# Kernel optimization log

Hardware: AMD Instinct MI355X
Metric: run time of the kernel (lower is better)

The kernel has to match this reference:

```python
import jax, jax.numpy as jnp
import numpy as np

N_NODES = 100000
N_EDGES = 3200000
D_FEAT = 128
HIDDEN = 128
BN_EPS = 1e-3  # Keras BatchNormalization default epsilon


def setup_inputs() -> dict:
    key = jax.random.key(0)
    k = jax.random.split(key, 8)
    H = jax.random.normal(k[0], (N_NODES, D_FEAT), dtype=jnp.float32)
    edge_src = jax.random.randint(k[1], (N_EDGES,), 0, N_NODES, dtype=jnp.int32)
    edge_dst = jax.random.randint(k[2], (N_EDGES,), 0, N_NODES, dtype=jnp.int32)
    edge_w = jax.random.uniform(k[3], (N_EDGES,), dtype=jnp.float32)
    # BatchNorm (inference-mode) parameters
    gamma = jnp.ones((D_FEAT,), dtype=jnp.float32)
    beta = jnp.zeros((D_FEAT,), dtype=jnp.float32)
    moving_mean = 0.1 * jax.random.normal(k[4], (D_FEAT,), dtype=jnp.float32)
    moving_var = jnp.abs(1.0 + 0.1 * jax.random.normal(k[5], (D_FEAT,), dtype=jnp.float32))
    # Dense layer params
    W = jax.random.normal(k[6], (D_FEAT, HIDDEN), dtype=jnp.float32) / np.sqrt(D_FEAT)
    b = jnp.zeros((HIDDEN,), dtype=jnp.float32)
    return {
        "H": H, "edge_src": edge_src, "edge_dst": edge_dst, "edge_w": edge_w,
        "gamma": gamma, "beta": beta, "moving_mean": moving_mean,
        "moving_var": moving_var, "W": W, "b": b, "num_nodes": N_NODES,
    }


def reference(H, edge_src, edge_dst, edge_w, gamma, beta, moving_mean, moving_var, W, b, num_nodes):
    # Sparse adjacency SpMM: h[dst] += w * H[src]
    msgs = H[edge_src] * edge_w[:, None]                      # [E, d]
    h = jax.ops.segment_sum(msgs, edge_dst, num_segments=num_nodes)  # [N, d]
    # BatchNorm (inference) -> Dropout (identity at inference) -> Dense + exact GELU
    h = (h - moving_mean) * jax.lax.rsqrt(moving_var + BN_EPS) * gamma + beta
    out = jax.nn.gelu(h @ W + b, approximate=False)           # [N, hidden]
    return out
```

## Files before the change

### kernel.cpp

```cpp
#include <hip/hip_runtime.h>
#include <math.h>


#define DF 128
#define SCAN_ELEMS 1024
#define BKSH 6
#define BKNODES (1 << BKSH)
#define NB 128
#define CAP 4096
#define CAP2 3072

typedef short short8 __attribute__((ext_vector_type(8)));
typedef float f32x4 __attribute__((ext_vector_type(4)));

__device__ __forceinline__ unsigned short f32_to_bf16_rne(float f) {
  unsigned u = __float_as_uint(f);
  return (unsigned short)((u + 0x7FFFu + ((u >> 16) & 1u)) >> 16);
}

__global__ __launch_bounds__(256) void scatter_kernel(
    const float* __restrict__ H, const int* __restrict__ esrc,
    const int* __restrict__ edst, const float* __restrict__ ew,
    float* __restrict__ h, int E) {
  int tid = blockIdx.x * blockDim.x + threadIdx.x;
  int e = tid >> 5;
  int lane = tid & 31;
  if (e >= E) return;
  int s = esrc[e];
  int d = edst[e];
  float w = ew[e];
  const float4* Hs = reinterpret_cast<const float4*>(H + (size_t)s * DF);
  float4 v = Hs[lane];
  float* hd = h + (size_t)d * DF + lane * 4;
  atomicAdd(hd + 0, v.x * w);
  atomicAdd(hd + 1, v.y * w);
  atomicAdd(hd + 2, v.z * w);
  atomicAdd(hd + 3, v.w * w);
}

__global__ __launch_bounds__(256) void prep_all_kernel(
    const float4* __restrict__ H4, ushort4* __restrict__ Hb, int n4,
    const float* __restrict__ W, const float* __restrict__ gamma,
    const float* __restrict__ beta, const float* __restrict__ mean,
    const float* __restrict__ var, const float* __restrict__ b,
    unsigned short* __restrict__ W2frag, float* __restrict__ bias2) {
  int idx = blockIdx.x * blockDim.x + threadIdx.x;
  if (idx < n4) {
    float4 v = H4[idx];
    ushort4 o;
    o.x = f32_to_bf16_rne(v.x);
    o.y = f32_to_bf16_rne(v.y);
    o.z = f32_to_bf16_rne(v.z);
    o.w = f32_to_bf16_rne(v.w);
    Hb[idx] = o;
  }
  if (idx < 16384) {
    int i = idx & 7;
    int l = (idx >> 3) & 63;
    int kt = (idx >> 9) & 3;
    int ct = idx >> 11;
    int k = kt * 32 + (l >> 4) * 8 + i;
    int c = ct * 16 + (l & 15);
    float s = gamma[k] * rsqrtf(var[k] + 1e-3f);
    W2frag[idx] = f32_to_bf16_rne(s * W[(size_t)k * DF + c]);
  } else if (idx < 16384 + DF) {
    int c = idx - 16384;
    float acc = b[c];
    for (int k = 0; k < DF; ++k) {
      float s = gamma[k] * rsqrtf(var[k] + 1e-3f);
      float t = beta[k] - mean[k] * s;
      acc += t * W[(size_t)k * DF + c];
    }
    bias2[c] = acc;
  }
}

__global__ __launch_bounds__(512) void hist_blk_kernel(
    const int* __restrict__ edst, int* __restrict__ bcnt,
    int E, int nbk, int chunk) {
  extern __shared__ int hcnt[];
  int bblk = blockIdx.x;
  int t = threadIdx.x;
  for (int i = t; i < nbk; i += 512) hcnt[i] = 0;
  __syncthreads();
  int e0 = bblk * chunk;
  int e1 = min(E, e0 + chunk);
  for (int e = e0 + t; e < e1; e += 512)
    atomicAdd(&hcnt[edst[e] >> BKSH], 1);
  __syncthreads();
  for (int k = t; k < nbk; k += 512)
    bcnt[(size_t)k * NB + bblk] = hcnt[k];
}

__global__ __launch_bounds__(256) void scan1_kernel(
    const int* __restrict__ cnt, int* __restrict__ pre,
    int* __restrict__ bsum, int N) {
  __shared__ int s[256];
  int t = threadIdx.x;
  int base = blockIdx.x * SCAN_ELEMS + t * 4;
  int v0 = (base + 0 < N) ? cnt[base + 0] : 0;
  int v1 = (base + 1 < N) ? cnt[base + 1] : 0;
  int v2 = (base + 2 < N) ? cnt[base + 2] : 0;
  int v3 = (base + 3 < N) ? cnt[base + 3] : 0;
  int tsum = v0 + v1 + v2 + v3;
  s[t] = tsum;
  __syncthreads();
  for (int off = 1; off < 256; off <<= 1) {
    int tmp = (t >= off) ? s[t - off] : 0;
    __syncthreads();
    s[t] += tmp;
    __syncthreads();
  }
  int run = s[t] - tsum;
  if (base + 0 < N) pre[base + 0] = run;
  run += v0;
  if (base + 1 < N) pre[base + 1] = run;
  run += v1;
  if (base + 2 < N) pre[base + 2] = run;
  run += v2;
  if (base + 3 < N) pre[base + 3] = run;
  if (t == 255) bsum[blockIdx.x] = s[255];
}

__global__ __launch_bounds__(256) void scan23_kernel(
    int* __restrict__ gbase, const int* __restrict__ bsum, int NBKG, int nbA) {
  __shared__ int s[256];
  int t = threadIdx.x;
  int v = (t < nbA) ? bsum[t] : 0;
  s[t] = v;
  __syncthreads();
  for (int off = 1; off < 256; off <<= 1) {
    int tmp = (t >= off) ? s[t - off] : 0;
    __syncthreads();
    s[t] += tmp;
    __syncthreads();
  }
  int i = blockIdx.x * 256 + t;
  if (i < NBKG) {
    int blk = i >> 10;
    int add = (blk == 0) ? 0 : s[blk - 1];
    gbase[i] += add;
  }
  if (blockIdx.x == 0 && t == 0) gbase[NBKG] = s[nbA - 1];
}

__global__ __launch_bounds__(512) void scatter_blk_kernel(
    const int* __restrict__ esrc, const int* __restrict__ edst,
    const float* __restrict__ ew, const int* __restrict__ gbase,
    uint2* __restrict__ payload, int E, int nbk, int chunk) {
  extern __shared__ int cur[];
  int bblk = blockIdx.x;
  int t = threadIdx.x;
  for (int k = t; k < nbk; k += 512) cur[k] = gbase[(size_t)k * NB + bblk];
  __syncthreads();
  int e0 = bblk * chunk;
  int e1 = min(E, e0 + chunk);
  for (int e = e0 + t; e < e1; e += 512) {
    int d = edst[e];
    int k = d >> BKSH;
    int pos = atomicAdd(&cur[k], 1);
    uint2 v;
    v.x = (unsigned)esrc[e] | ((unsigned)(d & (BKNODES - 1)) << 17);
    v.y = __float_as_uint(ew[e]);
    payload[pos] = v;
  }
}

__global__ __launch_bounds__(1024, 8) void reorder_pull_kernel(
    const unsigned* __restrict__ Hb, const uint2* __restrict__ payload,
    const int* __restrict__ gbase, unsigned* __restrict__ hb_out, int N) {
  __shared__ uint2 stage[CAP2];
  __shared__ uint2 sorted[CAP2];
  __shared__ int cnt[BKNODES];
  __shared__ int scn[BKNODES];
  __shared__ int cur[BKNODES];
  int bk = blockIdx.x;
  int t = threadIdx.x;
  int base = gbase[(size_t)bk * NB];
  int end  = gbase[(size_t)(bk + 1) * NB];
  int len = end - base;
  int wid = t >> 6;
  int lane = t & 63;

  if (len <= CAP2) {
    if (t < BKNODES) cnt[t] = 0;
    __syncthreads();
    for (int j = t; j < len; j += 1024) {
      uint2 m = payload[base + j];
      stage[j] = m;
      atomicAdd(&cnt[m.x >> 17], 1);
    }
    __syncthreads();
    if (t < BKNODES) scn[t] = cnt[t];
    __syncthreads();
    for (int off = 1; off < BKNODES; off <<= 1) {
      int tmp = 0;
      if (t < BKNODES && t >= off) tmp = scn[t - off];
      __syncthreads();
      if (t < BKNODES) scn[t] += tmp;
      __syncthreads();
    }
    if (t < BKNODES) cur[t] = scn[t] - cnt[t];
    __syncthreads();
    for (int j = t; j < len; j += 1024) {
      uint2 m = stage[j];
      int dl = (int)(m.x >> 17);
      int pos = atomicAdd(&cur[dl], 1);
      uint2 o;
      o.x = m.x & 0x1FFFFu;
      o.y = m.y;
      sorted[pos] = o;
    }
    __syncthreads();

#pragma unroll
    for (int i = 0; i < 4; ++i) {
      int dl = wid * 4 + i;
      int node = (bk << BKSH) + dl;
      if (node >= N) break;
      int s1 = scn[dl];
      int s0 = s1 - cnt[dl];
      float ax = 0.0f, ay = 0.0f;
      int j = s0;
      for (; j + 8 <= s1; j += 8) {
        uint2 m[8];
#pragma unroll
        for (int k = 0; k < 8; ++k) m[k] = sorted[j + k];
        float lo[8], hi[8];
#pragma unroll
        for (int k = 0; k < 8; ++k) {
          unsigned p = Hb[(size_t)m[k].x * 64 + lane];
          lo[k] = __uint_as_float(p << 16);
          hi[k] = __uint_as_float(p & 0xFFFF0000u);
        }
#pragma unroll
        for (int k = 0; k < 8; ++k) {
          float w = __uint_as_float(m[k].y);
          ax = fmaf(lo[k], w, ax);
          ay = fmaf(hi[k], w, ay);
        }
      }
      for (; j < s1; ++j) {
        uint2 m = sorted[j];
        float w = __uint_as_float(m.y);
        unsigned p = Hb[(size_t)m.x * 64 + lane];
        ax = fmaf(__uint_as_float(p << 16), w, ax);
        ay = fmaf(__uint_as_float(p & 0xFFFF0000u), w, ay);
      }
      unsigned pack = (unsigned)f32_to_bf16_rne(ax) |
                      ((unsigned)f32_to_bf16_rne(ay) << 16);
      hb_out[(size_t)node * 64 + lane] = pack;
    }
  } else {
#pragma unroll
    for (int i = 0; i < 4; ++i) {
      int dl = wid * 4 + i;
      int node = (bk << BKSH) + dl;
      if (node >= N) break;
      float ax = 0.0f, ay = 0.0f;
      for (int j = base; j < end; ++j) {
        uint2 m = payload[j];
        if ((int)(m.x >> 17) == dl) {
          float w = __uint_as_float(m.y);
          unsigned p = Hb[(size_t)(m.x & 0x1FFFFu) * 64 + lane];
          ax = fmaf(__uint_as_float(p << 16), w, ax);
          ay = fmaf(__uint_as_float(p & 0xFFFF0000u), w, ay);
        }
      }
      unsigned pack = (unsigned)f32_to_bf16_rne(ax) |
                      ((unsigned)f32_to_bf16_rne(ay) << 16);
      hb_out[(size_t)node * 64 + lane] = pack;
    }
  }
}

__global__ __launch_bounds__(256) void mfma_gemm_gelu_kernel(
    const unsigned short* __restrict__ hb,
    const unsigned short* __restrict__ W2frag,
    const float* __restrict__ bias2,
    float* __restrict__ out, int N) {
  __shared__ unsigned short sW[8 * 4 * 64 * 8];

  int t = threadIdx.x;
  {
    const uint4* src = (const uint4*)W2frag;
    uint4* dst = (uint4*)sW;
    for (int i = t; i < 2048; i += 256) dst[i] = src[i];
  }
  __syncthreads();

  int wid = t >> 6;
  int l = t & 63;
  int row0 = blockIdx.x * 64 + wid * 16;

  int arow = row0 + (l & 15);
  if (arow >= N) arow = N - 1;
  const short8* hrow = (const short8*)(hb + (size_t)arow * DF);
  int asub = l >> 4;
  short8 a[4];
#pragma unroll
  for (int kt = 0; kt < 4; ++kt) a[kt] = hrow[kt * 4 + asub];

  const short8* wf = (const short8*)sW;
  int orow = (l >> 4) * 4;
  int ocol = l & 15;

#pragma unroll
  for (int ct = 0; ct < 8; ++ct) {
    f32x4 acc = {0.0f, 0.0f, 0.0f, 0.0f};
#pragma unroll
    for (int kt = 0; kt < 4; ++kt) {
      short8 bfr = wf[(ct * 4 + kt) * 64 + l];
      acc = __builtin_amdgcn_mfma_f32_16x16x32_bf16(a[kt], bfr, acc, 0, 0, 0);
    }
    int col = ct * 16 + ocol;
    float bb = bias2[col];
#pragma unroll
    for (int r = 0; r < 4; ++r) {
      int row = row0 + orow + r;
      if (row < N) {
        float x = acc[r] + bb;
        float g = 0.5f * x * (1.0f + erff(x * 0.70710678118654752440f));
        out[(size_t)row * DF + col] = g;
      }
    }
  }
}

__global__ __launch_bounds__(256) void reorder2_kernel(
    const uint2* __restrict__ payload, const int* __restrict__ gbase,
    uint2* __restrict__ csr, int* __restrict__ rowptr,
    int N, int nbk, int E) {
  __shared__ uint2 stage[CAP];
  __shared__ int cnt[BKNODES];
  __shared__ int s64[BKNODES];
  __shared__ int cur[BKNODES];
  int bk = blockIdx.x;
  int t = threadIdx.x;
  int base = gbase[(size_t)bk * NB];
  int end  = gbase[(size_t)(bk + 1) * NB];
  int len = end - base;
  bool fit = (len <= CAP);

  if (t < BKNODES) cnt[t] = 0;
  __syncthreads();
  if (fit) {
    for (int j = t; j < len; j += 256) {
      uint2 m = payload[base + j];
      stage[j] = m;
      atomicAdd(&cnt[m.x >> 17], 1);
    }
  } else {
    for (int j = t; j < len; j += 256)
      atomicAdd(&cnt[payload[base + j].x >> 17], 1);
  }
  __syncthreads();
  if (t < BKNODES) s64[t] = cnt[t];
  __syncthreads();
  for (int off = 1; off < BKNODES; off <<= 1) {
    int tmp = 0;
    if (t < BKNODES && t >= off) tmp = s64[t - off];
    __syncthreads();
    if (t < BKNODES) s64[t] += tmp;
    __syncthreads();
  }
  if (t < BKNODES) {
    int ex = s64[t] - cnt[t];
    cur[t] = ex;
    int node = (bk << BKSH) + t;
    if (node < N) rowptr[node] = base + ex;
  }
  if (bk == nbk - 1 && t == 0) rowptr[N] = E;
  __syncthreads();
  if (fit) {
    for (int j = t; j < len; j += 256) {
      uint2 m = stage[j];
      int dl = (int)(m.x >> 17);
      int pos = atomicAdd(&cur[dl], 1);
      uint2 o;
      o.x = m.x & 0x1FFFFu;
      o.y = m.y;
      csr[(size_t)base + pos] = o;
    }
  } else {
    for (int j = t; j < len; j += 256) {
      uint2 m = payload[base + j];
      int dl = (int)(m.x >> 17);
      int pos = atomicAdd(&cur[dl], 1);
      uint2 o;
      o.x = m.x & 0x1FFFFu;
      o.y = m.y;
      csr[(size_t)base + pos] = o;
    }
  }
}

__global__ __launch_bounds__(256) void pull_csr_f32_kernel(
    const float2* __restrict__ H2, const int* __restrict__ rowptr,
    const uint2* __restrict__ csr_sw, float* __restrict__ h, int N) {
  int wave = threadIdx.x >> 6;
  int lane = threadIdx.x & 63;
  int node = blockIdx.x * 4 + wave;
  if (node >= N) return;
  int rs = rowptr[node];
  int re = rowptr[node + 1];
  float ax = 0.0f, ay = 0.0f;
  for (int j = rs; j < re; ++j) {
    uint2 m = csr_sw[j];
    float w = __uint_as_float(m.y);
    float2 u = H2[(size_t)m.x * 64 + lane];
    ax = fmaf(u.x, w, ax);
    ay = fmaf(u.y, w, ay);
  }
  float2 r;
  r.x = ax;
  r.y = ay;
  reinterpret_cast<float2*>(h)[(size_t)node * 64 + lane] = r;
}

__global__ __launch_bounds__(256) void fused_bn_gemm_gelu(
    float* __restrict__ hout, const float* __restrict__ gamma,
    const float* __restrict__ beta, const float* __restrict__ mean,
    const float* __restrict__ var, const float* __restrict__ W,
    const float* __restrict__ b, int N) {
  __shared__ float s_s[DF];
  __shared__ float s_t[DF];
  __shared__ float s_hb[16][DF];
  __shared__ float s_W[32][DF];

  int t = threadIdx.x;
  if (t < DF) {
    float sv = gamma[t] * rsqrtf(var[t] + 1e-3f);
    s_s[t] = sv;
    s_t[t] = beta[t] - mean[t] * sv;
  }
  __syncthreads();

  int n0 = blockIdx.x * 16;
  for (int i = t; i < 16 * DF; i += 256) {
    int r = i >> 7;
    int c = i & (DF - 1);
    int node = n0 + r;
    float hv = (node < N) ? hout[(size_t)node * DF + c] : 0.0f;
    s_hb[r][c] = hv * s_s[c] + s_t[c];
  }

  float acc[8];
#pragma unroll
  for (int i = 0; i < 8; i++) acc[i] = 0.0f;

  int col = t & (DF - 1);
  int half = t >> 7;

  for (int kc = 0; kc < DF; kc += 32) {
    __syncthreads();
    for (int i = t; i < 32 * DF; i += 256) {
      int r = i >> 7;
      int c = i & (DF - 1);
      s_W[r][c] = W[(size_t)(kc + r) * DF + c];
    }
    __syncthreads();
#pragma unroll
    for (int kk = 0; kk < 32; kk++) {
      float wv = s_W[kk][col];
#pragma unroll
      for (int i = 0; i < 8; i++) {
        acc[i] += s_hb[half + i * 2][kc + kk] * wv;
      }
    }
  }

  float bb = b[col];
#pragma unroll
  for (int i = 0; i < 8; i++) {
    int node = n0 + half + i * 2;
    if (node < N) {
      float x = acc[i] + bb;
      float g = 0.5f * x * (1.0f + erff(x * 0.70710678118654752440f));
      hout[(size_t)node * DF + col] = g;
    }
  }
}

extern "C" void kernel_launch(void* const* d_in, const int* in_sizes, int n_in,
                              void* d_out, int out_size, void* d_ws, size_t ws_size,
                              hipStream_t stream) {
  const float* H     = (const float*)d_in[0];
  const int*   esrc  = (const int*)d_in[1];
  const int*   edst  = (const int*)d_in[2];
  const float* ew    = (const float*)d_in[3];
  const float* gamma = (const float*)d_in[4];
  const float* beta  = (const float*)d_in[5];
  const float* mean  = (const float*)d_in[6];
  const float* var   = (const float*)d_in[7];
  const float* W     = (const float*)d_in[8];
  const float* b     = (const float*)d_in[9];

  int N = in_sizes[0] / DF;
  int E = in_sizes[1];
  float* h = (float*)d_out;

  int nbk = (N + BKNODES - 1) / BKNODES;
  int NBKG = nbk * NB;
  int nbA = (NBKG + SCAN_ELEMS - 1) / SCAN_ELEMS;
  int chunk = (E + NB - 1) / NB;

  size_t off = 0;
  auto alloc = [&](size_t bytes) {
    size_t o = off;
    off += (bytes + 255) & ~(size_t)255;
    return o;
  };
  size_t o_bcnt   = alloc((size_t)NBKG * 4);
  size_t o_gbase  = alloc((size_t)(NBKG + 1) * 4);
  size_t o_bsum   = alloc((size_t)(nbA + 1) * 4);
  size_t o_rowptr = alloc((size_t)(N + 1) * 4);
  size_t o_w2     = alloc((size_t)16384 * 2);
  size_t o_bias2  = alloc((size_t)DF * 4);
  size_t o_pl     = alloc((size_t)E * 8);
  size_t o_csr    = alloc((size_t)E * 8);
  size_t need_bin = off;
  size_t o_hb     = alloc((size_t)N * DF * 2);
  size_t need_bf16 = off;

  char* ws = (char*)d_ws;

  if (ws_size >= need_bin) {
    int* bcnt    = (int*)(ws + o_bcnt);
    int* gbase   = (int*)(ws + o_gbase);
    int* bsum    = (int*)(ws + o_bsum);
    int* rowptr  = (int*)(ws + o_rowptr);
    unsigned short* W2frag = (unsigned short*)(ws + o_w2);
    float* bias2 = (float*)(ws + o_bias2);
    uint2* payload = (uint2*)(ws + o_pl);
    uint2* csr     = (uint2*)(ws + o_csr);
    bool tierA = (ws_size >= need_bf16 && (size_t)N * DF * 2 <= (size_t)E * 8);

    size_t lds_bytes = (size_t)nbk * 4;

    if (tierA) {
      ushort4* Hb = (ushort4*)(ws + o_hb);
      int n4 = N * DF / 4;
      prep_all_kernel<<<(n4 + 255) / 256, 256, 0, stream>>>(
          (const float4*)H, Hb, n4, W, gamma, beta, mean, var, b, W2frag, bias2);
      hist_blk_kernel<<<NB, 512, lds_bytes, stream>>>(edst, bcnt, E, nbk, chunk);
      scan1_kernel<<<nbA, 256, 0, stream>>>(bcnt, gbase, bsum, NBKG);
      scan23_kernel<<<(NBKG + 255) / 256, 256, 0, stream>>>(gbase, bsum, NBKG, nbA);
      scatter_blk_kernel<<<NB, 512, lds_bytes, stream>>>(esrc, edst, ew, gbase,
                                                         payload, E, nbk, chunk);
      unsigned* hb_out = (unsigned*)(ws + o_csr);
      reorder_pull_kernel<<<nbk, 1024, 0, stream>>>(
          (const unsigned*)Hb, payload, gbase, hb_out, N);
      mfma_gemm_gelu_kernel<<<(N + 63) / 64, 256, 0, stream>>>(
          (const unsigned short*)hb_out, W2frag, bias2, (float*)d_out, N);
    } else {
      hist_blk_kernel<<<NB, 512, lds_bytes, stream>>>(edst, bcnt, E, nbk, chunk);
      scan1_kernel<<<nbA, 256, 0, stream>>>(bcnt, gbase, bsum, NBKG);
      scan23_kernel<<<(NBKG + 255) / 256, 256, 0, stream>>>(gbase, bsum, NBKG, nbA);
      scatter_blk_kernel<<<NB, 512, lds_bytes, stream>>>(esrc, edst, ew, gbase,
                                                         payload, E, nbk, chunk);
      reorder2_kernel<<<nbk, 256, 0, stream>>>(payload, gbase, csr, rowptr,
                                               N, nbk, E);
      pull_csr_f32_kernel<<<(N + 3) / 4, 256, 0, stream>>>(
          (const float2*)H, rowptr, csr, h, N);
      fused_bn_gemm_gelu<<<(N + 15) / 16, 256, 0, stream>>>(h, gamma, beta,
                                                            mean, var, W, b, N);
    }
  } else {
    hipMemsetAsync(d_out, 0, (size_t)out_size * sizeof(float), stream);
    long long threads = (long long)E * 32;
    long long grid = (threads + 255) / 256;
    scatter_kernel<<<(int)grid, 256, 0, stream>>>(H, esrc, edst, ew, h, E);
    fused_bn_gemm_gelu<<<(N + 15) / 16, 256, 0, stream>>>(h, gamma, beta,
                                                          mean, var, W, b, N);
  }
}
```

Measured before the change: 232.0 us.

## Persistent bucket-pull blocks, wider gather, in-place scan, and more binning blocks

The reorder+pull kernel becomes persistent: a fixed grid pulls bucket indices from a global atomic counter. It drops the LDS stage buffer and re-reads the payload from global memory instead. The gather now splits each wavefront into two half-waves that each load 8-byte bf16 chunks of alternating edges, then combines them with a cross-half shuffle. The binning uses 256 blocks instead of 128, the scan works in place with 8 elements per thread, and the GEMM processes two 64-row groups per block. Together these aim to cut LDS use, raise occupancy and memory-level parallelism, and shrink launch grids, at the cost of an extra memset and a second payload read.

```diff
diff --git a/kernel.cpp b/kernel.cpp
--- a/kernel.cpp
+++ b/kernel.cpp
@@ -3,12 +3,13 @@
 
 
 #define DF 128
-#define SCAN_ELEMS 1024
+#define SCAN_ELEMS 2048
 #define BKSH 6
 #define BKNODES (1 << BKSH)
-#define NB 128
+#define NB 256
 #define CAP 4096
 #define CAP2 3072
+#define PBLOCKS 512
 
 typedef short short8 __attribute__((ext_vector_type(8)));
 typedef float f32x4 __attribute__((ext_vector_type(4)));
@@ -76,7 +77,7 @@
 }
 
 __global__ __launch_bounds__(512) void hist_blk_kernel(
-    const int* __restrict__ edst, int* __restrict__ bcnt,
+    const int* __restrict__ edst, int* __restrict__ gbase,
     int E, int nbk, int chunk) {
   extern __shared__ int hcnt[];
   int bblk = blockIdx.x;
@@ -89,20 +90,21 @@
     atomicAdd(&hcnt[edst[e] >> BKSH], 1);
   __syncthreads();
   for (int k = t; k < nbk; k += 512)
-    bcnt[(size_t)k * NB + bblk] = hcnt[k];
+    gbase[(size_t)k * NB + bblk] = hcnt[k];
 }
 
 __global__ __launch_bounds__(256) void scan1_kernel(
-    const int* __restrict__ cnt, int* __restrict__ pre,
-    int* __restrict__ bsum, int N) {
+    int* __restrict__ data, int* __restrict__ bsum, int n) {
   __shared__ int s[256];
   int t = threadIdx.x;
-  int base = blockIdx.x * SCAN_ELEMS + t * 4;
-  int v0 = (base + 0 < N) ? cnt[base + 0] : 0;
-  int v1 = (base + 1 < N) ? cnt[base + 1] : 0;
-  int v2 = (base + 2 < N) ? cnt[base + 2] : 0;
-  int v3 = (base + 3 < N) ? cnt[base + 3] : 0;
-  int tsum = v0 + v1 + v2 + v3;
+  int base = blockIdx.x * SCAN_ELEMS + t * 8;
+  int v[8];
+  int tsum = 0;
+#pragma unroll
+  for (int k = 0; k < 8; ++k) {
+    v[k] = (base + k < n) ? data[base + k] : 0;
+    tsum += v[k];
+  }
   s[t] = tsum;
   __syncthreads();
   for (int off = 1; off < 256; off <<= 1) {
@@ -112,18 +114,16 @@
     __syncthreads();
   }
   int run = s[t] - tsum;
-  if (base + 0 < N) pre[base + 0] = run;
-  run += v0;
-  if (base + 1 < N) pre[base + 1] = run;
-  run += v1;
-  if (base + 2 < N) pre[base + 2] = run;
-  run += v2;
-  if (base + 3 < N) pre[base + 3] = run;
+#pragma unroll
+  for (int k = 0; k < 8; ++k) {
+    if (base + k < n) data[base + k] = run;
+    run += v[k];
+  }
   if (t == 255) bsum[blockIdx.x] = s[255];
 }
 
 __global__ __launch_bounds__(256) void scan23_kernel(
-    int* __restrict__ gbase, const int* __restrict__ bsum, int NBKG, int nbA) {
+    int* __restrict__ data, const int* __restrict__ bsum, int n, int nbA) {
   __shared__ int s[256];
   int t = threadIdx.x;
   int v = (t < nbA) ? bsum[t] : 0;
@@ -136,12 +136,12 @@
     __syncthreads();
   }
   int i = blockIdx.x * 256 + t;
-  if (i < NBKG) {
-    int blk = i >> 10;
+  if (i < n) {
+    int blk = i >> 11;
     int add = (blk == 0) ? 0 : s[blk - 1];
-    gbase[i] += add;
-  }
-  if (blockIdx.x == 0 && t == 0) gbase[NBKG] = s[nbA - 1];
+    data[i] += add;
+  }
+  if (blockIdx.x == 0 && t == 0) data[n] = s[nbA - 1];
 }
 
 __global__ __launch_bounds__(512) void scatter_blk_kernel(
@@ -168,109 +168,132 @@
 
 __global__ __launch_bounds__(1024, 8) void reorder_pull_kernel(
     const unsigned* __restrict__ Hb, const uint2* __restrict__ payload,
-    const int* __restrict__ gbase, unsigned* __restrict__ hb_out, int N) {
-  __shared__ uint2 stage[CAP2];
+    const int* __restrict__ gbase, unsigned* __restrict__ hb_out,
+    int* __restrict__ ctr, int N, int nbk) {
   __shared__ uint2 sorted[CAP2];
   __shared__ int cnt[BKNODES];
   __shared__ int scn[BKNODES];
   __shared__ int cur[BKNODES];
-  int bk = blockIdx.x;
-  int t = threadIdx.x;
-  int base = gbase[(size_t)bk * NB];
-  int end  = gbase[(size_t)(bk + 1) * NB];
-  int len = end - base;
+  __shared__ int s_bk;
+  int t = threadIdx.x;
   int wid = t >> 6;
   int lane = t & 63;
-
-  if (len <= CAP2) {
-    if (t < BKNODES) cnt[t] = 0;
-    __syncthreads();
-    for (int j = t; j < len; j += 1024) {
-      uint2 m = payload[base + j];
-      stage[j] = m;
-      atomicAdd(&cnt[m.x >> 17], 1);
-    }
-    __syncthreads();
-    if (t < BKNODES) scn[t] = cnt[t];
-    __syncthreads();
-    for (int off = 1; off < BKNODES; off <<= 1) {
-      int tmp = 0;
-      if (t < BKNODES && t >= off) tmp = scn[t - off];
+  int half = lane >> 5;
+  int sub = lane & 31;
+  const uint2* __restrict__ Hb2 = (const uint2*)Hb;
+
+  for (;;) {
+    if (t == 0) s_bk = atomicAdd(ctr, 1);
+    __syncthreads();
+    int bk = s_bk;
+    if (bk >= nbk) return;
+    int base = gbase[(size_t)bk * NB];
+    int end  = gbase[(size_t)(bk + 1) * NB];
+    int len = end - base;
+
+    if (len <= CAP2) {
+      if (t < BKNODES) cnt[t] = 0;
       __syncthreads();
-      if (t < BKNODES) scn[t] += tmp;
+      for (int j = t; j < len; j += 1024)
+        atomicAdd(&cnt[payload[base + j].x >> 17], 1);
       __syncthreads();
-    }
-    if (t < BKNODES) cur[t] = scn[t] - cnt[t];
-    __syncthreads();
-    for (int j = t; j < len; j += 1024) {
-      uint2 m = stage[j];
-      int dl = (int)(m.x >> 17);
-      int pos = atomicAdd(&cur[dl], 1);
-      uint2 o;
-      o.x = m.x & 0x1FFFFu;
-      o.y = m.y;
-      sorted[pos] = o;
-    }
-    __syncthreads();
-
-#pragma unroll
-    for (int i = 0; i < 4; ++i) {
-      int dl = wid * 4 + i;
-      int node = (bk << BKSH) + dl;
-      if (node >= N) break;
-      int s1 = scn[dl];
-      int s0 = s1 - cnt[dl];
-      float ax = 0.0f, ay = 0.0f;
-      int j = s0;
-      for (; j + 8 <= s1; j += 8) {
-        uint2 m[8];
-#pragma unroll
-        for (int k = 0; k < 8; ++k) m[k] = sorted[j + k];
-        float lo[8], hi[8];
-#pragma unroll
-        for (int k = 0; k < 8; ++k) {
-          unsigned p = Hb[(size_t)m[k].x * 64 + lane];
-          lo[k] = __uint_as_float(p << 16);
-          hi[k] = __uint_as_float(p & 0xFFFF0000u);
+      if (t < BKNODES) scn[t] = cnt[t];
+      __syncthreads();
+      for (int off = 1; off < BKNODES; off <<= 1) {
+        int tmp = (t < BKNODES && t >= off) ? scn[t - off] : 0;
+        __syncthreads();
+        if (t < BKNODES) scn[t] += tmp;
+        __syncthreads();
+      }
+      if (t < BKNODES) cur[t] = scn[t] - cnt[t];
+      __syncthreads();
+      for (int j = t; j < len; j += 1024) {
+        uint2 m = payload[base + j];
+        int pos = atomicAdd(&cur[m.x >> 17], 1);
+        uint2 o;
+        o.x = m.x & 0x1FFFFu;
+        o.y = m.y;
+        sorted[pos] = o;
+      }
+      __syncthreads();
+
+#pragma unroll
+      for (int i = 0; i < 4; ++i) {
+        int dl = wid * 4 + i;
+        int node = (bk << BKSH) + dl;
+        if (node >= N) break;
+        int s1 = scn[dl];
+        int s0 = s1 - cnt[dl];
+        float a0 = 0.0f, a1 = 0.0f, a2 = 0.0f, a3 = 0.0f;
+        int j = s0;
+        for (; j + 16 <= s1; j += 16) {
+          uint2 mm[8], rr[8];
+#pragma unroll
+          for (int k = 0; k < 8; ++k) mm[k] = sorted[j + 2 * k + half];
+#pragma unroll
+          for (int k = 0; k < 8; ++k)
+            rr[k] = Hb2[(size_t)mm[k].x * 32 + sub];
+#pragma unroll
+          for (int k = 0; k < 8; ++k) {
+            float w = __uint_as_float(mm[k].y);
+            a0 = fmaf(__uint_as_float(rr[k].x << 16), w, a0);
+            a1 = fmaf(__uint_as_float(rr[k].x & 0xFFFF0000u), w, a1);
+            a2 = fmaf(__uint_as_float(rr[k].y << 16), w, a2);
+            a3 = fmaf(__uint_as_float(rr[k].y & 0xFFFF0000u), w, a3);
+          }
         }
-#pragma unroll
-        for (int k = 0; k < 8; ++k) {
-          float w = __uint_as_float(m[k].y);
-          ax = fmaf(lo[k], w, ax);
-          ay = fmaf(hi[k], w, ay);
+        for (; j + 2 <= s1; j += 2) {
+          uint2 m = sorted[j + half];
+          uint2 r = Hb2[(size_t)m.x * 32 + sub];
+          float w = __uint_as_float(m.y);
+          a0 = fmaf(__uint_as_float(r.x << 16), w, a0);
+          a1 = fmaf(__uint_as_float(r.x & 0xFFFF0000u), w, a1);
+          a2 = fmaf(__uint_as_float(r.y << 16), w, a2);
+          a3 = fmaf(__uint_as_float(r.y & 0xFFFF0000u), w, a3);
+        }
+        if (j < s1 && half == 0) {
+          uint2 m = sorted[j];
+          uint2 r = Hb2[(size_t)m.x * 32 + sub];
+          float w = __uint_as_float(m.y);
+          a0 = fmaf(__uint_as_float(r.x << 16), w, a0);
+          a1 = fmaf(__uint_as_float(r.x & 0xFFFF0000u), w, a1);
+          a2 = fmaf(__uint_as_float(r.y << 16), w, a2);
+          a3 = fmaf(__uint_as_float(r.y & 0xFFFF0000u), w, a3);
+        }
+        a0 += __shfl_xor(a0, 32);
+        a1 += __shfl_xor(a1, 32);
+        a2 += __shfl_xor(a2, 32);
+        a3 += __shfl_xor(a3, 32);
+        if (half == 0) {
+          uint2 o;
+          o.x = (unsigned)f32_to_bf16_rne(a0) |
+                ((unsigned)f32_to_bf16_rne(a1) << 16);
+          o.y = (unsigned)f32_to_bf16_rne(a2) |
+                ((unsigned)f32_to_bf16_rne(a3) << 16);
+          ((uint2*)hb_out)[(size_t)node * 32 + sub] = o;
         }
       }
-      for (; j < s1; ++j) {
-        uint2 m = sorted[j];
-        float w = __uint_as_float(m.y);
-        unsigned p = Hb[(size_t)m.x * 64 + lane];
-        ax = fmaf(__uint_as_float(p << 16), w, ax);
-        ay = fmaf(__uint_as_float(p & 0xFFFF0000u), w, ay);
+    } else {
+      for (int i = 0; i < 4; ++i) {
+        int dl = wid * 4 + i;
+        int node = (bk << BKSH) + dl;
+        if (node >= N) break;
+        float ax = 0.0f, ay = 0.0f;
+        for (int j = base; j < end; ++j) {
+          uint2 m = payload[j];
+          if ((int)(m.x >> 17) == dl) {
+            float w = __uint_as_float(m.y);
+            unsigned p = Hb[(size_t)(m.x & 0x1FFFFu) * 64 + lane];
+            ax = fmaf(__uint_as_float(p << 16), w, ax);
+            ay = fmaf(__uint_as_float(p & 0xFFFF0000u), w, ay);
+          }
+        }
+        unsigned pack = (unsigned)f32_to_bf16_rne(ax) |
+                        ((unsigned)f32_to_bf16_rne(ay) << 16);
+        hb_out[(size_t)node * 64 + lane] = pack;
       }
-      unsigned pack = (unsigned)f32_to_bf16_rne(ax) |
-                      ((unsigned)f32_to_bf16_rne(ay) << 16);
-      hb_out[(size_t)node * 64 + lane] = pack;
-    }
-  } else {
-#pragma unroll
-    for (int i = 0; i < 4; ++i) {
-      int dl = wid * 4 + i;
-      int node = (bk << BKSH) + dl;
-      if (node >= N) break;
-      float ax = 0.0f, ay = 0.0f;
-      for (int j = base; j < end; ++j) {
-        uint2 m = payload[j];
-        if ((int)(m.x >> 17) == dl) {
-          float w = __uint_as_float(m.y);
-          unsigned p = Hb[(size_t)(m.x & 0x1FFFFu) * 64 + lane];
-          ax = fmaf(__uint_as_float(p << 16), w, ax);
-          ay = fmaf(__uint_as_float(p & 0xFFFF0000u), w, ay);
-        }
-      }
-      unsigned pack = (unsigned)f32_to_bf16_rne(ax) |
-                      ((unsigned)f32_to_bf16_rne(ay) << 16);
-      hb_out[(size_t)node * 64 + lane] = pack;
-    }
+    }
+    __syncthreads();
   }
 }
 
@@ -278,7 +301,7 @@
     const unsigned short* __restrict__ hb,
     const unsigned short* __restrict__ W2frag,
     const float* __restrict__ bias2,
-    float* __restrict__ out, int N) {
+    float* __restrict__ out, int N, int ngrp) {
   __shared__ unsigned short sW[8 * 4 * 64 * 8];
 
   int t = threadIdx.x;
@@ -291,37 +314,42 @@
 
   int wid = t >> 6;
   int l = t & 63;
-  int row0 = blockIdx.x * 64 + wid * 16;
-
-  int arow = row0 + (l & 15);
-  if (arow >= N) arow = N - 1;
-  const short8* hrow = (const short8*)(hb + (size_t)arow * DF);
-  int asub = l >> 4;
-  short8 a[4];
-#pragma unroll
-  for (int kt = 0; kt < 4; ++kt) a[kt] = hrow[kt * 4 + asub];
-
   const short8* wf = (const short8*)sW;
   int orow = (l >> 4) * 4;
   int ocol = l & 15;
 
 #pragma unroll
-  for (int ct = 0; ct < 8; ++ct) {
-    f32x4 acc = {0.0f, 0.0f, 0.0f, 0.0f};
-#pragma unroll
-    for (int kt = 0; kt < 4; ++kt) {
-      short8 bfr = wf[(ct * 4 + kt) * 64 + l];
-      acc = __builtin_amdgcn_mfma_f32_16x16x32_bf16(a[kt], bfr, acc, 0, 0, 0);
-    }
-    int col = ct * 16 + ocol;
-    float bb = bias2[col];
-#pragma unroll
-    for (int r = 0; r < 4; ++r) {
-      int row = row0 + orow + r;
-      if (row < N) {
-        float x = acc[r] + bb;
-        float g = 0.5f * x * (1.0f + erff(x * 0.70710678118654752440f));
-        out[(size_t)row * DF + col] = g;
+  for (int g = 0; g < 2; ++g) {
+    int grp = blockIdx.x * 2 + g;
+    if (grp >= ngrp) break;
+    int row0 = grp * 64 + wid * 16;
+
+    int arow = row0 + (l & 15);
+    if (arow >= N) arow = N - 1;
+    const short8* hrow = (const short8*)(hb + (size_t)arow * DF);
+    int asub = l >> 4;
+    short8 a[4];
+#pragma unroll
+    for (int kt = 0; kt < 4; ++kt) a[kt] = hrow[kt * 4 + asub];
+
+#pragma unroll
+    for (int ct = 0; ct < 8; ++ct) {
+      f32x4 acc = {0.0f, 0.0f, 0.0f, 0.0f};
+#pragma unroll
+      for (int kt = 0; kt < 4; ++kt) {
+        short8 bfr = wf[(ct * 4 + kt) * 64 + l];
+        acc = __builtin_amdgcn_mfma_f32_16x16x32_bf16(a[kt], bfr, acc, 0, 0, 0);
+      }
+      int col = ct * 16 + ocol;
+      float bb = bias2[col];
+#pragma unroll
+      for (int r = 0; r < 4; ++r) {
+        int row = row0 + orow + r;
+        if (row < N) {
+          float x = acc[r] + bb;
+          float gv = 0.5f * x * (1.0f + erff(x * 0.70710678118654752440f));
+          out[(size_t)row * DF + col] = gv;
+        }
       }
     }
   }
@@ -511,12 +539,12 @@
     off += (bytes + 255) & ~(size_t)255;
     return o;
   };
-  size_t o_bcnt   = alloc((size_t)NBKG * 4);
   size_t o_gbase  = alloc((size_t)(NBKG + 1) * 4);
   size_t o_bsum   = alloc((size_t)(nbA + 1) * 4);
   size_t o_rowptr = alloc((size_t)(N + 1) * 4);
   size_t o_w2     = alloc((size_t)16384 * 2);
   size_t o_bias2  = alloc((size_t)DF * 4);
+  size_t o_ctr    = alloc(256);
   size_t o_pl     = alloc((size_t)E * 8);
   size_t o_csr    = alloc((size_t)E * 8);
   size_t need_bin = off;
@@ -526,12 +554,12 @@
   char* ws = (char*)d_ws;
 
   if (ws_size >= need_bin) {
-    int* bcnt    = (int*)(ws + o_bcnt);
     int* gbase   = (int*)(ws + o_gbase);
     int* bsum    = (int*)(ws + o_bsum);
     int* rowptr  = (int*)(ws + o_rowptr);
     unsigned short* W2frag = (unsigned short*)(ws + o_w2);
     float* bias2 = (float*)(ws + o_bias2);
+    int* ctr     = (int*)(ws + o_ctr);
     uint2* payload = (uint2*)(ws + o_pl);
     uint2* csr     = (uint2*)(ws + o_csr);
     bool tierA = (ws_size >= need_bf16 && (size_t)N * DF * 2 <= (size_t)E * 8);
@@ -543,19 +571,22 @@
       int n4 = N * DF / 4;
       prep_all_kernel<<<(n4 + 255) / 256, 256, 0, stream>>>(
           (const float4*)H, Hb, n4, W, gamma, beta, mean, var, b, W2frag, bias2);
-      hist_blk_kernel<<<NB, 512, lds_bytes, stream>>>(edst, bcnt, E, nbk, chunk);
-      scan1_kernel<<<nbA, 256, 0, stream>>>(bcnt, gbase, bsum, NBKG);
+      hist_blk_kernel<<<NB, 512, lds_bytes, stream>>>(edst, gbase, E, nbk, chunk);
+      scan1_kernel<<<nbA, 256, 0, stream>>>(gbase, bsum, NBKG);
       scan23_kernel<<<(NBKG + 255) / 256, 256, 0, stream>>>(gbase, bsum, NBKG, nbA);
       scatter_blk_kernel<<<NB, 512, lds_bytes, stream>>>(esrc, edst, ew, gbase,
                                                          payload, E, nbk, chunk);
+      hipMemsetAsync(ctr, 0, 4, stream);
       unsigned* hb_out = (unsigned*)(ws + o_csr);
-      reorder_pull_kernel<<<nbk, 1024, 0, stream>>>(
-          (const unsigned*)Hb, payload, gbase, hb_out, N);
-      mfma_gemm_gelu_kernel<<<(N + 63) / 64, 256, 0, stream>>>(
-          (const unsigned short*)hb_out, W2frag, bias2, (float*)d_out, N);
+      int pgrid = min(PBLOCKS, nbk);
+      reorder_pull_kernel<<<pgrid, 1024, 0, stream>>>(
+          (const unsigned*)Hb, payload, gbase, hb_out, ctr, N, nbk);
+      int ngrp = (N + 63) / 64;
+      mfma_gemm_gelu_kernel<<<(ngrp + 1) / 2, 256, 0, stream>>>(
+          (const unsigned short*)hb_out, W2frag, bias2, (float*)d_out, N, ngrp);
     } else {
-      hist_blk_kernel<<<NB, 512, lds_bytes, stream>>>(edst, bcnt, E, nbk, chunk);
-      scan1_kernel<<<nbA, 256, 0, stream>>>(bcnt, gbase, bsum, NBKG);
+      hist_blk_kernel<<<NB, 512, lds_bytes, stream>>>(edst, gbase, E, nbk, chunk);
+      scan1_kernel<<<nbA, 256, 0, stream>>>(gbase, bsum, NBKG);
       scan23_kernel<<<(NBKG + 255) / 256, 256, 0, stream>>>(gbase, bsum, NBKG, nbA);
       scatter_blk_kernel<<<NB, 512, lds_bytes, stream>>>(esrc, edst, ew, gbase,
                                                          payload, E, nbk, chunk);
```

Result: slower. 247.8 us (+6.8%).
